# Optimization experiments

Measured on AMD Instinct MI355X. Metric: run time of the kernel, lower is better.

The kernel has to match this reference:

```python
import jax, jax.numpy as jnp
import numpy as np

B, N, DIM = 4, 4096, 512
HEADS, DH = 8, 64          # dim_head = dim // 8
M = 256                    # num_landmarks = dim // 2
ITERS = 6                  # pinv iterations
K = 33                     # residual depthwise conv kernel
INNER = HEADS * DH


def setup_inputs() -> dict:
    key = jax.random.key(0)
    ks = jax.random.split(key, 7)
    return {
        "x": jax.random.normal(ks[0], (B, N, DIM), jnp.float32),
        "norm_w": 1.0 + 0.02 * jax.random.normal(ks[1], (DIM,), jnp.float32),
        "norm_b": 0.02 * jax.random.normal(ks[2], (DIM,), jnp.float32),
        "w_qkv": jax.random.normal(ks[3], (DIM, 3 * INNER), jnp.float32) / np.sqrt(DIM),
        "w_out": jax.random.normal(ks[4], (INNER, DIM), jnp.float32) / np.sqrt(INNER),
        "b_out": 0.02 * jax.random.normal(ks[5], (DIM,), jnp.float32),
        "res_w": jax.random.normal(ks[6], (HEADS, 1, K, 1), jnp.float32) / np.sqrt(K),
    }


def _moore_penrose_pinv(x, iters):
    # iterative Newton-Schulz pseudoinverse, as in lucidrains nystrom-attention
    abs_x = jnp.abs(x)
    col = abs_x.sum(-1)
    row = abs_x.sum(-2)
    z = jnp.swapaxes(x, -1, -2) / (jnp.max(col) * jnp.max(row))
    I = jnp.eye(x.shape[-1], dtype=x.dtype)
    for _ in range(iters):
        xz = x @ z
        z = 0.25 * z @ (13.0 * I - xz @ (15.0 * I - xz @ (7.0 * I - xz)))
    return z


def reference(x, norm_w, norm_b, w_qkv, w_out, b_out, res_w):
    # LayerNorm (eps=1e-5, torch default)
    mu = x.mean(-1, keepdims=True)
    var = ((x - mu) ** 2).mean(-1, keepdims=True)
    xn = (x - mu) / jnp.sqrt(var + 1e-5) * norm_w + norm_b

    qkv = xn @ w_qkv                               # [B,N,3*INNER]
    q, k, v = jnp.split(qkv, 3, axis=-1)
    to_heads = lambda t: t.reshape(B, N, HEADS, DH).transpose(0, 2, 1, 3)  # [B,H,N,D]
    q, k, v = to_heads(q), to_heads(k), to_heads(v)
    q = q * (DH ** -0.5)

    # landmarks: mean over consecutive blocks of l = N // M tokens
    l = N // M
    q_l = q.reshape(B, HEADS, M, l, DH).mean(3)    # [B,H,M,D]
    k_l = k.reshape(B, HEADS, M, l, DH).mean(3)

    sim1 = jnp.einsum('bhid,bhjd->bhij', q, k_l)   # [B,H,N,M]
    sim2 = jnp.einsum('bhid,bhjd->bhij', q_l, k_l) # [B,H,M,M]
    sim3 = jnp.einsum('bhid,bhjd->bhij', q_l, k)   # [B,H,M,N]
    a1 = jax.nn.softmax(sim1, -1)
    a2 = jax.nn.softmax(sim2, -1)
    a3 = jax.nn.softmax(sim3, -1)

    a2_inv = _moore_penrose_pinv(a2, ITERS)
    out = (a1 @ a2_inv) @ (a3 @ v)                 # [B,H,N,D]

    # residual depthwise conv over sequence dim (Conv2d(h,h,(33,1),groups=h))
    out = out + jax.lax.conv_general_dilated(
        v, res_w, (1, 1), ((K // 2, K // 2), (0, 0)),
        feature_group_count=HEADS,
        dimension_numbers=('NCHW', 'OIHW', 'NCHW'))

    out = out.transpose(0, 2, 1, 3).reshape(B, N, INNER)
    out = out @ w_out + b_out                      # to_out (dropout inactive at eval)
    return x + out                                 # TransLayer residual
```

## Files before the change

kernel.cpp:

```cpp
#include <hip/hip_runtime.h>
#include <math.h>

typedef unsigned short u16;
typedef short s16x8 __attribute__((ext_vector_type(8)));
typedef float f32x4 __attribute__((ext_vector_type(4)));

#define MFMA16(a, b, c) __builtin_amdgcn_mfma_f32_16x16x32_bf16((a), (b), (c), 0, 0, 0)

__device__ __forceinline__ u16 f2b(float f) {
  unsigned u = __float_as_uint(f);
  unsigned r = (u + 0x7fff + ((u >> 16) & 1)) >> 16;
  return (u16)r;
}
__device__ __forceinline__ float b2f(u16 h) { return __uint_as_float(((unsigned)h) << 16); }

__global__ __launch_bounds__(256) void prep_kernel(const float* __restrict__ x, const float* __restrict__ w,
    const float* __restrict__ b, u16* __restrict__ xn,
    const float* __restrict__ Wq, u16* __restrict__ WqT,
    const float* __restrict__ Wo, u16* __restrict__ WoT,
    unsigned* __restrict__ scal) {
  int bI = blockIdx.x;
  int t = threadIdx.x;
  if (bI == 0 && t == 0) { scal[0] = 0u; scal[1] = 0u; }
  if (bI < 16384) {
    int row = bI;
    const float* xr = x + (size_t)row * 512;
    float v0 = xr[t], v1 = xr[t + 256];
    float s = v0 + v1, ss = v0*v0 + v1*v1;
    for (int o = 32; o > 0; o >>= 1) { s += __shfl_down(s, o); ss += __shfl_down(ss, o); }
    __shared__ float ls[4], lss[4];
    int wid = t >> 6, lane = t & 63;
    if (lane == 0) { ls[wid] = s; lss[wid] = ss; }
    __syncthreads();
    float tot  = ls[0]+ls[1]+ls[2]+ls[3];
    float tot2 = lss[0]+lss[1]+lss[2]+lss[3];
    float mean = tot * (1.f/512);
    float var  = tot2 * (1.f/512) - mean*mean;
    float inv = rsqrtf(var + 1e-5f);
    u16* xo = xn + (size_t)row * 512;
    xo[t]     = f2b((v0-mean)*inv*w[t]     + b[t]);
    xo[t+256] = f2b((v1-mean)*inv*w[t+256] + b[t+256]);
  } else if (bI < 16384 + 3072) {
    int idx = (bI - 16384)*256 + t;
    int r = idx / 1536, c = idx - r*1536;
    WqT[(size_t)c*512 + r] = f2b(Wq[idx]);
  } else {
    int idx = (bI - 19456)*256 + t;
    int r = idx >> 9, c = idx & 511;
    WoT[(size_t)c*512 + r] = f2b(Wo[idx]);
  }
}

__device__ __forceinline__ void gemm128_pf(const u16* __restrict__ A, const u16* __restrict__ BT,
    int K, int ldA, int ldBT, int row0, int col0, u16* As, u16* Bs, f32x4 acc[4][4]) {
  int t = threadIdx.x, lane = t & 63, wid = t >> 6;
  int wr = (wid >> 1) * 64, wc = (wid & 1) * 64;
  int lr = lane & 15, lg = lane >> 4;
  int sr = t >> 2, sc = (t & 3) * 8;
  const u16* Ar0 = A  + (size_t)(row0 + sr)*ldA + sc;
  const u16* Ar1 = A  + (size_t)(row0 + sr + 64)*ldA + sc;
  const u16* Br0 = BT + (size_t)(col0 + sr)*ldBT + sc;
  const u16* Br1 = BT + (size_t)(col0 + sr + 64)*ldBT + sc;
  uint4 pa0 = *(const uint4*)Ar0, pa1 = *(const uint4*)Ar1;
  uint4 pb0 = *(const uint4*)Br0, pb1 = *(const uint4*)Br1;
  for (int k0 = 0; k0 < K; k0 += 32) {
    __syncthreads();
    *(uint4*)&As[sr*40 + sc]        = pa0;
    *(uint4*)&As[(sr + 64)*40 + sc] = pa1;
    *(uint4*)&Bs[sr*40 + sc]        = pb0;
    *(uint4*)&Bs[(sr + 64)*40 + sc] = pb1;
    __syncthreads();
    if (k0 + 32 < K) {
      pa0 = *(const uint4*)(Ar0 + k0 + 32);
      pa1 = *(const uint4*)(Ar1 + k0 + 32);
      pb0 = *(const uint4*)(Br0 + k0 + 32);
      pb1 = *(const uint4*)(Br1 + k0 + 32);
    }
    s16x8 af[4], bf[4];
    #pragma unroll
    for (int f = 0; f < 4; f++) {
      af[f] = *(s16x8*)&As[(wr + f*16 + lr)*40 + lg*8];
      bf[f] = *(s16x8*)&Bs[(wc + f*16 + lr)*40 + lg*8];
    }
    #pragma unroll
    for (int i = 0; i < 4; i++)
      #pragma unroll
      for (int j = 0; j < 4; j++)
        acc[i][j] = MFMA16(af[i], bf[j], acc[i][j]);
  }
}

__device__ __forceinline__ void gemm64_pf(const u16* __restrict__ Ab, const u16* __restrict__ Bb,
    int row0, int col0, u16* As, u16* Bs, f32x4 acc[2][2]) {
  int t = threadIdx.x, lane = t & 63, wid = t >> 6;
  int wr = (wid >> 1)*32, wc = (wid & 1)*32;
  int lr = lane & 15, lg = lane >> 4;
  int sr = t >> 3, sc = (t & 7)*8;
  const u16* Ar0 = Ab + (size_t)(row0 + sr)*256 + sc;
  const u16* Ar1 = Ab + (size_t)(row0 + 32 + sr)*256 + sc;
  const u16* Br0 = Bb + (size_t)(col0 + sr)*256 + sc;
  const u16* Br1 = Bb + (size_t)(col0 + 32 + sr)*256 + sc;
  uint4 pa0 = *(const uint4*)Ar0, pa1 = *(const uint4*)Ar1;
  uint4 pb0 = *(const uint4*)Br0, pb1 = *(const uint4*)Br1;
  for (int k0 = 0; k0 < 256; k0 += 64) {
    __syncthreads();
    *(uint4*)&As[sr*72 + sc]        = pa0;
    *(uint4*)&As[(sr + 32)*72 + sc] = pa1;
    *(uint4*)&Bs[sr*72 + sc]        = pb0;
    *(uint4*)&Bs[(sr + 32)*72 + sc] = pb1;
    __syncthreads();
    if (k0 + 64 < 256) {
      pa0 = *(const uint4*)(Ar0 + k0 + 64);
      pa1 = *(const uint4*)(Ar1 + k0 + 64);
      pb0 = *(const uint4*)(Br0 + k0 + 64);
      pb1 = *(const uint4*)(Br1 + k0 + 64);
    }
    #pragma unroll
    for (int kk = 0; kk < 2; kk++) {
      s16x8 af[2], bf[2];
      #pragma unroll
      for (int f = 0; f < 2; f++) {
        af[f] = *(s16x8*)&As[(wr + f*16 + lr)*72 + kk*32 + lg*8];
        bf[f] = *(s16x8*)&Bs[(wc + f*16 + lr)*72 + kk*32 + lg*8];
      }
      #pragma unroll
      for (int i = 0; i < 2; i++)
        #pragma unroll
        for (int j = 0; j < 2; j++)
          acc[i][j] = MFMA16(af[i], bf[j], acc[i][j]);
    }
  }
}

__global__ __launch_bounds__(256, 4) void qkv_mfma(const u16* __restrict__ xn, const u16* __restrict__ wT,
    u16* __restrict__ q, u16* __restrict__ k, u16* __restrict__ v,
    u16* __restrict__ ql, u16* __restrict__ kl) {
  __shared__ u16 As[128*40], Bs[128*40];
  f32x4 acc[4][4];
  #pragma unroll
  for (int i = 0; i < 4; i++)
    #pragma unroll
    for (int j = 0; j < 4; j++) acc[i][j] = (f32x4)0.f;
  int bI = blockIdx.x;
  int job = (bI & 7)*192 + (bI >> 3);
  int row0 = (job / 12) * 128, col0 = (job % 12) * 128;
  gemm128_pf(xn, wT, 512, 512, 512, row0, col0, As, Bs, acc);
  int t = threadIdx.x, lane = t & 63, wid = t >> 6, lr = lane & 15, lg = lane >> 4;
  int wr = (wid >> 1)*64, wc = (wid & 1)*64;
  int part = col0 >> 9;
  #pragma unroll
  for (int i = 0; i < 4; i++)
    #pragma unroll
    for (int j = 0; j < 4; j++)
      #pragma unroll
      for (int r = 0; r < 4; r++) {
        int row = row0 + wr + i*16 + lg*4 + r;
        int col = col0 + wc + j*16 + lr;
        float val = acc[i][j][r];
        int rem = col & 511, h = rem >> 6, d = rem & 63;
        int b = row >> 12, n = row & 4095;
        size_t bh = (size_t)(b*8 + h);
        size_t dst = (bh*4096 + n)*64 + d;
        if (part == 0)      q[dst] = f2b(val * 0.125f);
        else if (part == 1) k[dst] = f2b(val);
        else                v[dst] = f2b(val);
      }
  if (part <= 1) {
    #pragma unroll
    for (int i = 0; i < 4; i++) {
      #pragma unroll
      for (int j = 0; j < 4; j++) {
        float s = acc[i][j][0] + acc[i][j][1] + acc[i][j][2] + acc[i][j][3];
        s += __shfl_xor(s, 16);
        s += __shfl_xor(s, 32);
        if (lg == 0) {
          int row16 = row0 + wr + i*16;
          int b = row16 >> 12, n = row16 & 4095;
          int m = n >> 4;
          int col = col0 + wc + j*16 + lr;
          int rem = col & 511, h = rem >> 6, d = rem & 63;
          size_t dst = ((size_t)(b*8 + h)*256 + m)*64 + d;
          if (part == 0) ql[dst] = f2b(s * (0.125f/16.f));
          else           kl[dst] = f2b(s * (1.f/16.f));
        }
      }
    }
  }
}

__global__ __launch_bounds__(256, 4) void out_mfma(const u16* __restrict__ outh, const u16* __restrict__ wT,
    const float* __restrict__ bo, const float* __restrict__ x, float* __restrict__ out) {
  __shared__ u16 As[128*40], Bs[128*40];
  f32x4 acc[4][4];
  #pragma unroll
  for (int i = 0; i < 4; i++)
    #pragma unroll
    for (int j = 0; j < 4; j++) acc[i][j] = (f32x4)0.f;
  int bI = blockIdx.x;
  int job = (bI & 7)*64 + (bI >> 3);
  int row0 = (job / 4) * 128, col0 = (job % 4) * 128;
  gemm128_pf(outh, wT, 512, 512, 512, row0, col0, As, Bs, acc);
  int t = threadIdx.x, lane = t & 63, wid = t >> 6, lr = lane & 15, lg = lane >> 4;
  int wr = (wid >> 1)*64, wc = (wid & 1)*64;
  #pragma unroll
  for (int i = 0; i < 4; i++)
    #pragma unroll
    for (int j = 0; j < 4; j++)
      #pragma unroll
      for (int r = 0; r < 4; r++) {
        int row = row0 + wr + i*16 + lg*4 + r;
        int col = col0 + wc + j*16 + lr;
        size_t idx = (size_t)row*512 + col;
        out[idx] = x[idx] + acc[i][j][r] + bo[col];
      }
}

__global__ __launch_bounds__(256) void mid_kernel(
    const u16* __restrict__ v, u16* __restrict__ vT,
    const u16* __restrict__ ql, const u16* __restrict__ kl,
    u16* __restrict__ a2h, float* __restrict__ pcs,
    const float* __restrict__ rw, u16* __restrict__ outh) {
  __shared__ __align__(16) u16 smem[25600];
  int bI = blockIdx.x;
  int t = threadIdx.x;
  if (bI < 128) {
    int rq = bI & 3, bh = bI >> 2;
    u16* Qs  = smem;
    u16* Ks2 = smem + 4608;
    float* wcol = (float*)(smem + 23040);
    int lane = t & 63, wid = t >> 6, lr = lane & 15, lg = lane >> 4;
    #pragma unroll
    for (int p = 0; p < 2; p++) {
      int c = t + p*256;
      int r = c >> 3, col = (c & 7)*8;
      *(uint4*)&Qs[r*72 + col] = *(const uint4*)&ql[((size_t)bh*256 + rq*64 + r)*64 + col];
    }
    #pragma unroll
    for (int p = 0; p < 8; p++) {
      int c = t + p*256;
      int r = c >> 3, col = (c & 7)*8;
      *(uint4*)&Ks2[r*72 + col] = *(const uint4*)&kl[((size_t)bh*256 + r)*64 + col];
    }
    __syncthreads();
    float colp[16];
    #pragma unroll
    for (int cf = 0; cf < 16; cf++) colp[cf] = 0.f;
    int rbase = wid*16;
    s16x8 a0 = *(s16x8*)&Qs[(rbase + lr)*72 + lg*8];
    s16x8 a1 = *(s16x8*)&Qs[(rbase + lr)*72 + 32 + lg*8];
    f32x4 sf[16];
    #pragma unroll
    for (int cf = 0; cf < 16; cf++) {
      s16x8 b0 = *(s16x8*)&Ks2[(cf*16 + lr)*72 + lg*8];
      s16x8 b1 = *(s16x8*)&Ks2[(cf*16 + lr)*72 + 32 + lg*8];
      sf[cf] = MFMA16(a1, b1, MFMA16(a0, b0, (f32x4)0.f));
    }
    #pragma unroll
    for (int r = 0; r < 4; r++) {
      float mx = -3e38f;
      #pragma unroll
      for (int cf = 0; cf < 16; cf++) mx = fmaxf(mx, sf[cf][r]);
      #pragma unroll
      for (int o = 1; o < 16; o <<= 1) mx = fmaxf(mx, __shfl_xor(mx, o));
      float sum = 0.f;
      #pragma unroll
      for (int cf = 0; cf < 16; cf++) { sf[cf][r] = __expf(sf[cf][r] - mx); sum += sf[cf][r]; }
      #pragma unroll
      for (int o = 1; o < 16; o <<= 1) sum += __shfl_xor(sum, o);
      float inv = 1.f / sum;
      int row = rq*64 + rbase + lg*4 + r;
      size_t base = (size_t)bh*65536 + (size_t)row*256;
      #pragma unroll
      for (int cf = 0; cf < 16; cf++) {
        float pp = sf[cf][r] * inv;
        a2h[base + cf*16 + lr] = f2b(pp);
        colp[cf] += pp;
      }
    }
    #pragma unroll
    for (int cf = 0; cf < 16; cf++) {
      colp[cf] += __shfl_xor(colp[cf], 16);
      colp[cf] += __shfl_xor(colp[cf], 32);
    }
    if (lg == 0) {
      #pragma unroll
      for (int cf = 0; cf < 16; cf++) wcol[wid*256 + cf*16 + lr] = colp[cf];
    }
    __syncthreads();
    pcs[((size_t)bh*4 + rq)*256 + t] = wcol[t] + wcol[256 + t] + wcol[512 + t] + wcol[768 + t];
  } else if (bI < 2176) {
    int idx = bI - 128;
    int bh = idx >> 6, n0 = (idx & 63) * 64;
    u16* tile = smem;
    const u16* vb = v + ((size_t)bh*4096 + n0)*64;
    #pragma unroll
    for (int p = 0; p < 2; p++) {
      int c = t + p*256;
      int r = c >> 3, col = (c & 7)*8;
      *(uint4*)&tile[r*72 + col] = *(const uint4*)&vb[(size_t)r*64 + col];
    }
    __syncthreads();
    #pragma unroll
    for (int p = 0; p < 2; p++) {
      int c = t + p*256;
      int d = c >> 3, ncol = (c & 7)*8;
      u16 tmp[8];
      #pragma unroll
      for (int j = 0; j < 8; j++) tmp[j] = tile[(ncol + j)*72 + d];
      *(uint4*)&vT[((size_t)bh*64 + d)*4096 + n0 + ncol] = *(uint4*)tmp;
    }
  } else {
    int idx = bI - 2176;
    int bh = idx >> 5, n0 = (idx & 31) * 128;
    int b = bh >> 3, h = bh & 7;
    u16* tile = smem;
    float* wsm = (float*)(smem + 11520);
    if (t < 33) wsm[t] = rw[h*33 + t];
    const u16* vb = v + ((size_t)bh*4096)*64;
    #pragma unroll
    for (int p = 0; p < 5; p++) {
      int c = t + p*256;
      int r = c >> 3, col = (c & 7)*8;
      int nn = n0 - 16 + r;
      uint4 val = make_uint4(0u,0u,0u,0u);
      if (nn >= 0 && nn < 4096) val = *(const uint4*)&vb[(size_t)nn*64 + col];
      *(uint4*)&tile[r*72 + col] = val;
    }
    __syncthreads();
    int d8 = (t & 7) * 8;
    int r0 = t >> 3;
    #pragma unroll
    for (int pass = 0; pass < 4; pass++) {
      int lrow = pass*32 + r0;
      float acc[8] = {};
      #pragma unroll
      for (int j = 0; j < 33; j++) {
        uint4 vv = *(uint4*)&tile[(lrow + j)*72 + d8];
        float w = wsm[j];
        acc[0] += b2f((u16)(vv.x & 0xffff)) * w;
        acc[1] += b2f((u16)(vv.x >> 16))    * w;
        acc[2] += b2f((u16)(vv.y & 0xffff)) * w;
        acc[3] += b2f((u16)(vv.y >> 16))    * w;
        acc[4] += b2f((u16)(vv.z & 0xffff)) * w;
        acc[5] += b2f((u16)(vv.z >> 16))    * w;
        acc[6] += b2f((u16)(vv.w & 0xffff)) * w;
        acc[7] += b2f((u16)(vv.w >> 16))    * w;
      }
      size_t oi = ((size_t)(b*4096 + n0 + lrow))*512 + h*64 + d8;
      uint4 nv;
      nv.x = (unsigned)f2b(acc[0]) | ((unsigned)f2b(acc[1]) << 16);
      nv.y = (unsigned)f2b(acc[2]) | ((unsigned)f2b(acc[3]) << 16);
      nv.z = (unsigned)f2b(acc[4]) | ((unsigned)f2b(acc[5]) << 16);
      nv.w = (unsigned)f2b(acc[6]) | ((unsigned)f2b(acc[7]) << 16);
      *(uint4*)&outh[oi] = nv;
    }
  }
}

__global__ __launch_bounds__(256) void colmax_kernel(const float* __restrict__ pcs, unsigned* __restrict__ scal) {
  __shared__ float red[256];
  int bh = blockIdx.x, t = threadIdx.x;
  size_t b4 = (size_t)bh*4*256;
  red[t] = pcs[b4 + t] + pcs[b4 + 256 + t] + pcs[b4 + 512 + t] + pcs[b4 + 768 + t];
  __syncthreads();
  for (int o = 128; o > 0; o >>= 1) {
    if (t < o) red[t] = fmaxf(red[t], red[t+o]);
    __syncthreads();
  }
  if (t == 0) atomicMax(scal + 1, __float_as_uint(red[0]));
}

__global__ __launch_bounds__(256) void flash_part(const u16* __restrict__ Q, const u16* __restrict__ Kg,
    const u16* __restrict__ VT, u16* __restrict__ po, float* __restrict__ pl) {
  __shared__ u16 Ks[64*72];
  __shared__ u16 Vs[64*72];
  __shared__ u16 Ps[4*16*72];
  int ch = blockIdx.x, qg = blockIdx.y, bh = blockIdx.z;
  int t = threadIdx.x, lane = t & 63, wid = t >> 6, lr = lane & 15, lg = lane >> 4;
  const u16* Qb  = Q  + ((size_t)bh*256)*64;
  const u16* Kb  = Kg + ((size_t)bh*4096 + ch*512)*64;
  const u16* VTb = VT + ((size_t)bh*64)*4096 + ch*512;
  s16x8 aq[2][2];
  #pragma unroll
  for (int qq = 0; qq < 2; qq++) {
    int qrow = (qg*2 + qq)*64 + wid*16 + lr;
    aq[qq][0] = *(const s16x8*)&Qb[(size_t)qrow*64 + lg*8];
    aq[qq][1] = *(const s16x8*)&Qb[(size_t)qrow*64 + 32 + lg*8];
  }
  f32x4 oacc[2][4];
  f32x4 lacc[2];
  #pragma unroll
  for (int qq = 0; qq < 2; qq++) {
    lacc[qq] = (f32x4)0.f;
    #pragma unroll
    for (int f = 0; f < 4; f++) oacc[qq][f] = (f32x4)0.f;
  }
  u16* Pw = Ps + wid*16*72;
  uint4 pk[2], pv[2];
  #pragma unroll
  for (int p = 0; p < 2; p++) {
    int c = t + p*256; int r = c >> 3, cc = (c & 7)*8;
    pk[p] = *(const uint4*)&Kb[(size_t)r*64 + cc];
    pv[p] = *(const uint4*)&VTb[(size_t)r*4096 + cc];
  }
  for (int k0 = 0; k0 < 512; k0 += 64) {
    __syncthreads();
    #pragma unroll
    for (int p = 0; p < 2; p++) {
      int c = t + p*256; int r = c >> 3, cc = (c & 7)*8;
      *(uint4*)&Ks[r*72 + cc] = pk[p];
      *(uint4*)&Vs[r*72 + cc] = pv[p];
    }
    __syncthreads();
    if (k0 + 64 < 512) {
      #pragma unroll
      for (int p = 0; p < 2; p++) {
        int c = t + p*256; int r = c >> 3, cc = (c & 7)*8;
        pk[p] = *(const uint4*)&Kb[(size_t)(k0 + 64 + r)*64 + cc];
        pv[p] = *(const uint4*)&VTb[(size_t)r*4096 + k0 + 64 + cc];
      }
    }
    #pragma unroll
    for (int qq = 0; qq < 2; qq++) {
      f32x4 sf[4];
      #pragma unroll
      for (int f = 0; f < 4; f++) {
        s16x8 b0 = *(s16x8*)&Ks[(f*16 + lr)*72 + lg*8];
        s16x8 b1 = *(s16x8*)&Ks[(f*16 + lr)*72 + 32 + lg*8];
        f32x4 s = (f32x4)0.f;
        s = MFMA16(aq[qq][0], b0, s);
        s = MFMA16(aq[qq][1], b1, s);
        sf[f] = s;
      }
      #pragma unroll
      for (int r = 0; r < 4; r++) {
        #pragma unroll
        for (int f = 0; f < 4; f++) {
          float pv2 = __expf(sf[f][r] - 8.f);
          lacc[qq][r] += pv2;
          Pw[(lg*4 + r)*72 + f*16 + lr] = f2b(pv2);
        }
      }
      #pragma unroll
      for (int ks = 0; ks < 2; ks++) {
        s16x8 ap = *(s16x8*)&Pw[lr*72 + ks*32 + lg*8];
        #pragma unroll
        for (int df = 0; df < 4; df++) {
          s16x8 bv = *(s16x8*)&Vs[(df*16 + lr)*72 + ks*32 + lg*8];
          oacc[qq][df] = MFMA16(ap, bv, oacc[qq][df]);
        }
      }
    }
  }
  #pragma unroll
  for (int qq = 0; qq < 2; qq++) {
    #pragma unroll
    for (int r = 0; r < 4; r++) {
      float s = lacc[qq][r];
      #pragma unroll
      for (int o = 1; o < 16; o <<= 1) s += __shfl_xor(s, o);
      lacc[qq][r] = s;
    }
  }
  #pragma unroll
  for (int qq = 0; qq < 2; qq++) {
    int pidx = (bh*4 + qg*2 + qq)*8 + ch;
    #pragma unroll
    for (int r = 0; r < 4; r++) {
      int lrow = wid*16 + lg*4 + r;
      if (lr == 0) pl[pidx*64 + lrow] = lacc[qq][r];
      uint2 pw2;
      pw2.x = (unsigned)f2b(oacc[qq][0][r]) | ((unsigned)f2b(oacc[qq][1][r]) << 16);
      pw2.y = (unsigned)f2b(oacc[qq][2][r]) | ((unsigned)f2b(oacc[qq][3][r]) << 16);
      *(uint2*)&po[((size_t)pidx*64 + lrow)*64 + lr*4] = pw2;
    }
  }
}

__global__ __launch_bounds__(256) void merge_z0(const u16* __restrict__ po,
    const float* __restrict__ pl, u16* __restrict__ a3vT,
    const u16* __restrict__ a2h, const unsigned* __restrict__ scal,
    u16* __restrict__ zA, u16* __restrict__ zAT) {
  __shared__ u16 tile[64*72];
  int bI = blockIdx.x;
  int t = threadIdx.x;
  if (bI < 128) {
    int qt = bI & 3, bh = bI >> 2;
    int lrow = t & 63, dg = t >> 6;
    int pbase = (bh*4 + qt)*8;
    float L = 0.f;
    #pragma unroll
    for (int ch = 0; ch < 8; ch++) L += pl[(pbase+ch)*64 + lrow];
    float Oacc[16];
    #pragma unroll
    for (int ss = 0; ss < 16; ss++) Oacc[ss] = 0.f;
    #pragma unroll
    for (int ch = 0; ch < 8; ch++) {
      const u16* pr = &po[(((size_t)(pbase+ch)*64 + lrow)*64) + dg*16];
      uint4 v0 = *(const uint4*)pr;
      uint4 v1 = *(const uint4*)(pr + 8);
      unsigned arr[8] = {v0.x, v0.y, v0.z, v0.w, v1.x, v1.y, v1.z, v1.w};
      #pragma unroll
      for (int jj = 0; jj < 8; jj++) {
        Oacc[jj*2]   += b2f((u16)(arr[jj] & 0xffff));
        Oacc[jj*2+1] += b2f((u16)(arr[jj] >> 16));
      }
    }
    float Linv = 1.f / L;
    #pragma unroll
    for (int ss = 0; ss < 16; ss++) {
      int s = dg*16 + ss;
      int c = ((s & 3) << 4) | (s >> 2);
      tile[c*72 + lrow] = f2b(Oacc[ss] * Linv);
    }
    __syncthreads();
    #pragma unroll
    for (int p = 0; p < 2; p++) {
      int idx = t + p*256;
      int d = idx >> 3, seg = idx & 7;
      u16 tmp[8];
      #pragma unroll
      for (int j = 0; j < 8; j++) tmp[j] = tile[d*72 + seg*8 + j];
      *(uint4*)&a3vT[((size_t)bh*64 + d)*256 + qt*64 + seg*8] = *(uint4*)tmp;
    }
  } else {
    size_t idx = (size_t)(bI - 128)*256 + t;
    float inv = 1.f / __uint_as_float(scal[1]);
    size_t bh = idx >> 16; int rem = (int)(idx & 65535); int i = rem >> 8, j = rem & 255;
    zA[idx]  = f2b(b2f(a2h[(bh<<16) + ((size_t)j<<8) + i]) * inv);
    zAT[idx] = f2b(b2f(a2h[idx]) * inv);
  }
}

__global__ __launch_bounds__(256) void pinv_s1(const u16* __restrict__ a2h, const u16* __restrict__ zcT,
    u16* __restrict__ xz, u16* __restrict__ xzT, u16* __restrict__ e1T) {
  __shared__ u16 As[64*72], Bs[64*72];
  size_t bb = (size_t)blockIdx.z << 16;
  f32x4 acc[2][2];
  #pragma unroll
  for (int i = 0; i < 2; i++) { acc[i][0] = (f32x4)0.f; acc[i][1] = (f32x4)0.f; }
  int row0 = blockIdx.y*64, col0 = blockIdx.x*64;
  gemm64_pf(a2h + bb, zcT + bb, row0, col0, As, Bs, acc);
  int t = threadIdx.x, lane = t & 63, wid = t >> 6, lr = lane & 15, lg = lane >> 4;
  int wr = (wid >> 1)*32, wc = (wid & 1)*32;
  #pragma unroll
  for (int i = 0; i < 2; i++)
    #pragma unroll
    for (int j = 0; j < 2; j++)
      #pragma unroll
      for (int r = 0; r < 4; r++) {
        int row = row0 + wr + i*16 + lg*4 + r;
        int col = col0 + wc + j*16 + lr;
        float c = acc[i][j][r];
        xz [bb + (size_t)row*256 + col] = f2b(c);
        xzT[bb + (size_t)col*256 + row] = f2b(c);
        e1T[bb + (size_t)col*256 + row] = f2b((row == col ? 7.f : 0.f) - c);
      }
}

__global__ __launch_bounds__(256) void pinv_s2(const u16* __restrict__ xz, const u16* __restrict__ e1T,
    const u16* __restrict__ zc, const u16* __restrict__ xzT,
    u16* __restrict__ e2T, u16* __restrict__ W) {
  __shared__ u16 As[64*72], Bs[64*72];
  int bz = blockIdx.z;
  bool isQ = bz < 32;
  size_t bb = (size_t)(isQ ? bz : bz - 32) << 16;
  const u16* Aptr = (isQ ? xz : zc) + bb;
  const u16* Bptr = (isQ ? e1T : xzT) + bb;
  f32x4 acc[2][2];
  #pragma unroll
  for (int i = 0; i < 2; i++) { acc[i][0] = (f32x4)0.f; acc[i][1] = (f32x4)0.f; }
  int row0 = blockIdx.y*64, col0 = blockIdx.x*64;
  gemm64_pf(Aptr, Bptr, row0, col0, As, Bs, acc);
  int t = threadIdx.x, lane = t & 63, wid = t >> 6, lr = lane & 15, lg = lane >> 4;
  int wr = (wid >> 1)*32, wc = (wid & 1)*32;
  #pragma unroll
  for (int i = 0; i < 2; i++)
    #pragma unroll
    for (int j = 0; j < 2; j++)
      #pragma unroll
      for (int r = 0; r < 4; r++) {
        int row = row0 + wr + i*16 + lg*4 + r;
        int col = col0 + wc + j*16 + lr;
        float c = acc[i][j][r];
        if (isQ) e2T[bb + (size_t)col*256 + row] = f2b((row == col ? 15.f : 0.f) - c);
        else     W  [bb + (size_t)row*256 + col] = f2b(c);
      }
}

__global__ __launch_bounds__(256) void pinv_s3(const u16* __restrict__ W, const u16* __restrict__ e2T,
    const u16* __restrict__ zc, u16* __restrict__ zn, u16* __restrict__ znT) {
  __shared__ u16 As[64*72], Bs[64*72];
  size_t bb = (size_t)blockIdx.z << 16;
  f32x4 acc[2][2];
  #pragma unroll
  for (int i = 0; i < 2; i++) { acc[i][0] = (f32x4)0.f; acc[i][1] = (f32x4)0.f; }
  int row0 = blockIdx.y*64, col0 = blockIdx.x*64;
  gemm64_pf(W + bb, e2T + bb, row0, col0, As, Bs, acc);
  int t = threadIdx.x, lane = t & 63, wid = t >> 6, lr = lane & 15, lg = lane >> 4;
  int wr = (wid >> 1)*32, wc = (wid & 1)*32;
  #pragma unroll
  for (int i = 0; i < 2; i++)
    #pragma unroll
    for (int j = 0; j < 2; j++)
      #pragma unroll
      for (int r = 0; r < 4; r++) {
        int row = row0 + wr + i*16 + lg*4 + r;
        int col = col0 + wc + j*16 + lr;
        size_t idx = bb + (size_t)row*256 + col;
        float val = 3.25f*b2f(zc[idx]) - 0.25f*acc[i][j][r];
        zn [idx] = f2b(val);
        znT[bb + (size_t)col*256 + row] = f2b(val);
      }
}

__global__ __launch_bounds__(256) void bmm64(const u16* __restrict__ A, const u16* __restrict__ BT,
    u16* __restrict__ CT, int M, int N, int K) {
  __shared__ u16 As[64*40], Bs[64*40];
  int batch = blockIdx.z;
  const u16* Ab = A  + (size_t)batch*M*K;
  const u16* Bb = BT + (size_t)batch*N*K;
  int row0 = blockIdx.y*64, col0 = blockIdx.x*64;
  int t = threadIdx.x, lane = t & 63, wid = t >> 6, lr = lane & 15, lg = lane >> 4;
  int wr = (wid >> 1)*32, wc = (wid & 1)*32;
  int sr = t >> 2, sc = (t & 3)*8;
  const u16* Arow = Ab + (size_t)(row0 + sr)*K + sc;
  const u16* Brow = Bb + (size_t)(col0 + sr)*K + sc;
  uint4 pa = *(const uint4*)Arow;
  uint4 pb = *(const uint4*)Brow;
  f32x4 acc[2][2];
  #pragma unroll
  for (int i = 0; i < 2; i++)
    #pragma unroll
    for (int j = 0; j < 2; j++) acc[i][j] = (f32x4)0.f;
  for (int k0 = 0; k0 < K; k0 += 32) {
    __syncthreads();
    *(uint4*)&As[sr*40 + sc] = pa;
    *(uint4*)&Bs[sr*40 + sc] = pb;
    __syncthreads();
    if (k0 + 32 < K) {
      pa = *(const uint4*)(Arow + k0 + 32);
      pb = *(const uint4*)(Brow + k0 + 32);
    }
    s16x8 af[2], bf[2];
    #pragma unroll
    for (int f = 0; f < 2; f++) {
      af[f] = *(s16x8*)&As[(wr + f*16 + lr)*40 + lg*8];
      bf[f] = *(s16x8*)&Bs[(wc + f*16 + lr)*40 + lg*8];
    }
    #pragma unroll
    for (int i = 0; i < 2; i++)
      #pragma unroll
      for (int j = 0; j < 2; j++)
        acc[i][j] = MFMA16(af[i], bf[j], acc[i][j]);
  }
  size_t cb = (size_t)batch*M*N;
  #pragma unroll
  for (int i = 0; i < 2; i++)
    #pragma unroll
    for (int j = 0; j < 2; j++)
      #pragma unroll
      for (int r = 0; r < 4; r++) {
        int row = row0 + wr + i*16 + lg*4 + r;
        int col = col0 + wc + j*16 + lr;
        CT[cb + (size_t)col*M + row] = f2b(acc[i][j][r]);
      }
}

__global__ __launch_bounds__(256, 4) void flash_a1(const u16* __restrict__ Q, const u16* __restrict__ Kl,
    const u16* __restrict__ W2T, u16* __restrict__ outh) {
  __shared__ u16 Ks[64*72];
  __shared__ u16 Vs[64*264];
  __shared__ u16 Ps[4*16*264];
  int bh = blockIdx.y;
  int q0 = blockIdx.x * 64;
  int t = threadIdx.x, lane = t & 63, wid = t >> 6, lr = lane & 15, lg = lane >> 4;
  const u16* Qb = Q + ((size_t)bh*4096)*64;
  #pragma unroll
  for (int p = 0; p < 8; p++) {
    int c = t + p*256; int r = c >> 5, col = (c & 31)*8;
    *(uint4*)&Vs[r*264 + col] = *(const uint4*)&W2T[((size_t)bh*64 + r)*256 + col];
  }
  int qrow = q0 + wid*16 + lr;
  s16x8 aq0 = *(const s16x8*)&Qb[(size_t)qrow*64 + lg*8];
  s16x8 aq1 = *(const s16x8*)&Qb[(size_t)qrow*64 + 32 + lg*8];
  f32x4 sf[16];
  #pragma unroll
  for (int f = 0; f < 16; f++) sf[f] = (f32x4)0.f;
  #pragma unroll
  for (int kt = 0; kt < 4; kt++) {
    __syncthreads();
    #pragma unroll
    for (int p = 0; p < 2; p++) {
      int c = t + p*256; int r = c >> 3, cc = (c & 7)*8;
      *(uint4*)&Ks[r*72 + cc] = *(const uint4*)&Kl[((size_t)bh*256 + kt*64 + r)*64 + cc];
    }
    __syncthreads();
    #pragma unroll
    for (int f2 = 0; f2 < 4; f2++) {
      s16x8 b0 = *(s16x8*)&Ks[(f2*16 + lr)*72 + lg*8];
      s16x8 b1 = *(s16x8*)&Ks[(f2*16 + lr)*72 + 32 + lg*8];
      sf[kt*4 + f2] = MFMA16(aq1, b1, MFMA16(aq0, b0, sf[kt*4 + f2]));
    }
  }
  u16* Pw = Ps + wid*16*264;
  float linv[4];
  #pragma unroll
  for (int r = 0; r < 4; r++) {
    float sum = 0.f;
    #pragma unroll
    for (int f = 0; f < 16; f++) {
      float pv = __expf(sf[f][r] - 8.f);
      sum += pv;
      Pw[(lg*4 + r)*264 + f*16 + lr] = f2b(pv);
    }
    #pragma unroll
    for (int o = 1; o < 16; o <<= 1) sum += __shfl_xor(sum, o);
    linv[r] = 1.f / sum;
  }
  f32x4 oacc[4];
  #pragma unroll
  for (int f = 0; f < 4; f++) oacc[f] = (f32x4)0.f;
  #pragma unroll
  for (int ks = 0; ks < 8; ks++) {
    s16x8 ap = *(s16x8*)&Pw[lr*264 + ks*32 + lg*8];
    #pragma unroll
    for (int df = 0; df < 4; df++) {
      s16x8 bv = *(s16x8*)&Vs[(df*16 + lr)*264 + ks*32 + lg*8];
      oacc[df] = MFMA16(ap, bv, oacc[df]);
    }
  }
  int b = bh >> 3, h = bh & 7;
  #pragma unroll
  for (int df = 0; df < 4; df++)
    #pragma unroll
    for (int r = 0; r < 4; r++) {
      int lrow = wid*16 + lg*4 + r;
      int col = df*16 + lr;
      size_t oi = ((size_t)(b*4096 + q0 + lrow))*512 + h*64 + col;
      outh[oi] = f2b(b2f(outh[oi]) + oacc[df][r] * linv[r]);
    }
}

extern "C" void kernel_launch(void* const* d_in, const int* in_sizes, int n_in,
                              void* d_out, int out_size, void* d_ws, size_t ws_size,
                              hipStream_t stream) {
  const float* x      = (const float*)d_in[0];
  const float* norm_w = (const float*)d_in[1];
  const float* norm_b = (const float*)d_in[2];
  const float* w_qkv  = (const float*)d_in[3];
  const float* w_out  = (const float*)d_in[4];
  const float* b_out  = (const float*)d_in[5];
  const float* res_w  = (const float*)d_in[6];
  float* out = (float*)d_out;
  char* ws = (char*)d_ws;

  size_t off = 0;
  u16* xn    = (u16*)(ws + off); off += 16777216;
  u16* q     = (u16*)(ws + off); off += 16777216;
  u16* k     = (u16*)(ws + off); off += 16777216;
  u16* v     = (u16*)(ws + off); off += 16777216;
  u16* vT    = (u16*)(ws + off); off += 16777216;
  u16* ql    = (u16*)(ws + off); off += 1048576;
  u16* kl    = (u16*)(ws + off); off += 1048576;
  u16* a2h   = (u16*)(ws + off); off += 4194304;
  u16* zA    = (u16*)(ws + off); off += 4194304;
  u16* zAT   = (u16*)(ws + off); off += 4194304;
  u16* zB    = (u16*)(ws + off); off += 4194304;
  u16* zBT   = (u16*)(ws + off); off += 4194304;
  u16* xz    = (u16*)(ws + off); off += 4194304;
  u16* xzT   = (u16*)(ws + off); off += 4194304;
  u16* e1T   = (u16*)(ws + off); off += 4194304;
  u16* e2T   = (u16*)(ws + off); off += 4194304;
  u16* Wm    = (u16*)(ws + off); off += 4194304;
  u16* a3vT  = (u16*)(ws + off); off += 1048576;
  u16* w2T   = (u16*)(ws + off); off += 1048576;
  u16* wqkvT = (u16*)(ws + off); off += 1572864;
  u16* woutT = (u16*)(ws + off); off += 524288;
  u16* outh  = (u16*)(ws + off); off += 16777216;
  u16* po    = (u16*)(ws + off); off += 8388608;
  float* pl  = (float*)(ws + off); off += 262144;
  float* pcs = (float*)(ws + off); off += 131072;
  unsigned* scal = (unsigned*)(ws + off); off += 8;

  prep_kernel<<<20480, 256, 0, stream>>>(x, norm_w, norm_b, xn, w_qkv, wqkvT, w_out, woutT, scal);
  qkv_mfma<<<1536, 256, 0, stream>>>(xn, wqkvT, q, k, v, ql, kl);
  mid_kernel<<<3200, 256, 0, stream>>>(v, vT, ql, kl, a2h, pcs, res_w, outh);
  colmax_kernel<<<32, 256, 0, stream>>>(pcs, scal);
  flash_part<<<dim3(8, 2, 32), 256, 0, stream>>>(ql, k, vT, po, pl);
  merge_z0<<<8320, 256, 0, stream>>>(po, pl, a3vT, a2h, scal, zA, zAT);

  u16 *zc = zA, *zcT = zAT, *zn = zB, *znT = zBT;
  for (int it = 0; it < 6; it++) {
    pinv_s1<<<dim3(4,4,32), 256, 0, stream>>>(a2h, zcT, xz, xzT, e1T);
    pinv_s2<<<dim3(4,4,64), 256, 0, stream>>>(xz, e1T, zc, xzT, e2T, Wm);
    pinv_s3<<<dim3(4,4,32), 256, 0, stream>>>(Wm, e2T, zc, zn, znT);
    u16* tp;
    tp = zc; zc = zn; zn = tp;
    tp = zcT; zcT = znT; znT = tp;
  }

  bmm64<<<dim3(1,4,32), 256, 0, stream>>>(zc, a3vT, w2T, 256, 64, 256);
  flash_a1<<<dim3(64, 32), 256, 0, stream>>>(q, kl, w2T, outh);
  out_mfma<<<512, 256, 0, stream>>>(outh, woutT, b_out, x, out);
}
```

Measured before the change: 384.5 us.

## Load full K panel in one pass for 64x64 GEMMs and fuse colmax into flash_part

The 64x64 GEMM helper used by the pinv stages and bmm64 now loads the entire 256-wide K panel into shared memory in one pass behind a single barrier. This replaces the register-prefetched loop that synchronised on every K chunk. The colmax reduction is folded into the flash_part launch as extra blocks, removing one kernel launch. The trade-off is about 67 KB of shared memory per block, which lowers occupancy and leaves no overlap between the loads and the MFMA work.

```diff
diff --git a/kernel.cpp b/kernel.cpp
--- a/kernel.cpp
+++ b/kernel.cpp
@@ -90,45 +90,32 @@
   }
 }
 
-__device__ __forceinline__ void gemm64_pf(const u16* __restrict__ Ab, const u16* __restrict__ Bb,
+__device__ __forceinline__ void gemm64_1p(const u16* __restrict__ Ab, const u16* __restrict__ Bb,
     int row0, int col0, u16* As, u16* Bs, f32x4 acc[2][2]) {
   int t = threadIdx.x, lane = t & 63, wid = t >> 6;
   int wr = (wid >> 1)*32, wc = (wid & 1)*32;
   int lr = lane & 15, lg = lane >> 4;
-  int sr = t >> 3, sc = (t & 7)*8;
-  const u16* Ar0 = Ab + (size_t)(row0 + sr)*256 + sc;
-  const u16* Ar1 = Ab + (size_t)(row0 + 32 + sr)*256 + sc;
-  const u16* Br0 = Bb + (size_t)(col0 + sr)*256 + sc;
-  const u16* Br1 = Bb + (size_t)(col0 + 32 + sr)*256 + sc;
-  uint4 pa0 = *(const uint4*)Ar0, pa1 = *(const uint4*)Ar1;
-  uint4 pb0 = *(const uint4*)Br0, pb1 = *(const uint4*)Br1;
-  for (int k0 = 0; k0 < 256; k0 += 64) {
-    __syncthreads();
-    *(uint4*)&As[sr*72 + sc]        = pa0;
-    *(uint4*)&As[(sr + 32)*72 + sc] = pa1;
-    *(uint4*)&Bs[sr*72 + sc]        = pb0;
-    *(uint4*)&Bs[(sr + 32)*72 + sc] = pb1;
-    __syncthreads();
-    if (k0 + 64 < 256) {
-      pa0 = *(const uint4*)(Ar0 + k0 + 64);
-      pa1 = *(const uint4*)(Ar1 + k0 + 64);
-      pb0 = *(const uint4*)(Br0 + k0 + 64);
-      pb1 = *(const uint4*)(Br1 + k0 + 64);
-    }
-    #pragma unroll
-    for (int kk = 0; kk < 2; kk++) {
-      s16x8 af[2], bf[2];
-      #pragma unroll
-      for (int f = 0; f < 2; f++) {
-        af[f] = *(s16x8*)&As[(wr + f*16 + lr)*72 + kk*32 + lg*8];
-        bf[f] = *(s16x8*)&Bs[(wc + f*16 + lr)*72 + kk*32 + lg*8];
-      }
-      #pragma unroll
-      for (int i = 0; i < 2; i++)
-        #pragma unroll
-        for (int j = 0; j < 2; j++)
-          acc[i][j] = MFMA16(af[i], bf[j], acc[i][j]);
-    }
+  #pragma unroll
+  for (int p = 0; p < 8; p++) {
+    int idx = t + p*256;
+    int r = idx >> 5, c = (idx & 31)*8;
+    *(uint4*)&As[r*264 + c] = *(const uint4*)&Ab[(size_t)(row0 + r)*256 + c];
+    *(uint4*)&Bs[r*264 + c] = *(const uint4*)&Bb[(size_t)(col0 + r)*256 + c];
+  }
+  __syncthreads();
+  #pragma unroll
+  for (int kk = 0; kk < 8; kk++) {
+    s16x8 af[2], bf[2];
+    #pragma unroll
+    for (int f = 0; f < 2; f++) {
+      af[f] = *(s16x8*)&As[(wr + f*16 + lr)*264 + kk*32 + lg*8];
+      bf[f] = *(s16x8*)&Bs[(wc + f*16 + lr)*264 + kk*32 + lg*8];
+    }
+    #pragma unroll
+    for (int i = 0; i < 2; i++)
+      #pragma unroll
+      for (int j = 0; j < 2; j++)
+        acc[i][j] = MFMA16(af[i], bf[j], acc[i][j]);
   }
 }
 
@@ -357,26 +344,30 @@
   }
 }
 
-__global__ __launch_bounds__(256) void colmax_kernel(const float* __restrict__ pcs, unsigned* __restrict__ scal) {
-  __shared__ float red[256];
-  int bh = blockIdx.x, t = threadIdx.x;
-  size_t b4 = (size_t)bh*4*256;
-  red[t] = pcs[b4 + t] + pcs[b4 + 256 + t] + pcs[b4 + 512 + t] + pcs[b4 + 768 + t];
-  __syncthreads();
-  for (int o = 128; o > 0; o >>= 1) {
-    if (t < o) red[t] = fmaxf(red[t], red[t+o]);
-    __syncthreads();
-  }
-  if (t == 0) atomicMax(scal + 1, __float_as_uint(red[0]));
-}
-
-__global__ __launch_bounds__(256) void flash_part(const u16* __restrict__ Q, const u16* __restrict__ Kg,
-    const u16* __restrict__ VT, u16* __restrict__ po, float* __restrict__ pl) {
-  __shared__ u16 Ks[64*72];
-  __shared__ u16 Vs[64*72];
-  __shared__ u16 Ps[4*16*72];
-  int ch = blockIdx.x, qg = blockIdx.y, bh = blockIdx.z;
-  int t = threadIdx.x, lane = t & 63, wid = t >> 6, lr = lane & 15, lg = lane >> 4;
+__global__ __launch_bounds__(256) void fp_cm(const u16* __restrict__ Q, const u16* __restrict__ Kg,
+    const u16* __restrict__ VT, u16* __restrict__ po, float* __restrict__ pl,
+    const float* __restrict__ pcs, unsigned* __restrict__ scal) {
+  __shared__ __align__(16) u16 smem[13824];
+  int bI = blockIdx.x;
+  int t = threadIdx.x;
+  if (bI >= 512) {
+    float* red = (float*)smem;
+    int bh = bI - 512;
+    size_t b4 = (size_t)bh*4*256;
+    red[t] = pcs[b4 + t] + pcs[b4 + 256 + t] + pcs[b4 + 512 + t] + pcs[b4 + 768 + t];
+    __syncthreads();
+    for (int o = 128; o > 0; o >>= 1) {
+      if (t < o) red[t] = fmaxf(red[t], red[t+o]);
+      __syncthreads();
+    }
+    if (t == 0) atomicMax(scal + 1, __float_as_uint(red[0]));
+    return;
+  }
+  int ch = bI & 7, qg = (bI >> 3) & 1, bh = bI >> 4;
+  u16* Ks = smem;
+  u16* Vs = smem + 4608;
+  u16* Ps = smem + 9216;
+  int lane = t & 63, wid = t >> 6, lr = lane & 15, lg = lane >> 4;
   const u16* Qb  = Q  + ((size_t)bh*256)*64;
   const u16* Kb  = Kg + ((size_t)bh*4096 + ch*512)*64;
   const u16* VTb = VT + ((size_t)bh*64)*4096 + ch*512;
@@ -534,13 +525,13 @@
 
 __global__ __launch_bounds__(256) void pinv_s1(const u16* __restrict__ a2h, const u16* __restrict__ zcT,
     u16* __restrict__ xz, u16* __restrict__ xzT, u16* __restrict__ e1T) {
-  __shared__ u16 As[64*72], Bs[64*72];
+  __shared__ u16 As[64*264], Bs[64*264];
   size_t bb = (size_t)blockIdx.z << 16;
   f32x4 acc[2][2];
   #pragma unroll
   for (int i = 0; i < 2; i++) { acc[i][0] = (f32x4)0.f; acc[i][1] = (f32x4)0.f; }
   int row0 = blockIdx.y*64, col0 = blockIdx.x*64;
-  gemm64_pf(a2h + bb, zcT + bb, row0, col0, As, Bs, acc);
+  gemm64_1p(a2h + bb, zcT + bb, row0, col0, As, Bs, acc);
   int t = threadIdx.x, lane = t & 63, wid = t >> 6, lr = lane & 15, lg = lane >> 4;
   int wr = (wid >> 1)*32, wc = (wid & 1)*32;
   #pragma unroll
@@ -561,7 +552,7 @@
 __global__ __launch_bounds__(256) void pinv_s2(const u16* __restrict__ xz, const u16* __restrict__ e1T,
     const u16* __restrict__ zc, const u16* __restrict__ xzT,
     u16* __restrict__ e2T, u16* __restrict__ W) {
-  __shared__ u16 As[64*72], Bs[64*72];
+  __shared__ u16 As[64*264], Bs[64*264];
   int bz = blockIdx.z;
   bool isQ = bz < 32;
   size_t bb = (size_t)(isQ ? bz : bz - 32) << 16;
@@ -571,7 +562,7 @@
   #pragma unroll
   for (int i = 0; i < 2; i++) { acc[i][0] = (f32x4)0.f; acc[i][1] = (f32x4)0.f; }
   int row0 = blockIdx.y*64, col0 = blockIdx.x*64;
-  gemm64_pf(Aptr, Bptr, row0, col0, As, Bs, acc);
+  gemm64_1p(Aptr, Bptr, row0, col0, As, Bs, acc);
   int t = threadIdx.x, lane = t & 63, wid = t >> 6, lr = lane & 15, lg = lane >> 4;
   int wr = (wid >> 1)*32, wc = (wid & 1)*32;
   #pragma unroll
@@ -590,13 +581,13 @@
 
 __global__ __launch_bounds__(256) void pinv_s3(const u16* __restrict__ W, const u16* __restrict__ e2T,
     const u16* __restrict__ zc, u16* __restrict__ zn, u16* __restrict__ znT) {
-  __shared__ u16 As[64*72], Bs[64*72];
+  __shared__ u16 As[64*264], Bs[64*264];
   size_t bb = (size_t)blockIdx.z << 16;
   f32x4 acc[2][2];
   #pragma unroll
   for (int i = 0; i < 2; i++) { acc[i][0] = (f32x4)0.f; acc[i][1] = (f32x4)0.f; }
   int row0 = blockIdx.y*64, col0 = blockIdx.x*64;
-  gemm64_pf(W + bb, e2T + bb, row0, col0, As, Bs, acc);
+  gemm64_1p(W + bb, e2T + bb, row0, col0, As, Bs, acc);
   int t = threadIdx.x, lane = t & 63, wid = t >> 6, lr = lane & 15, lg = lane >> 4;
   int wr = (wid >> 1)*32, wc = (wid & 1)*32;
   #pragma unroll
@@ -616,44 +607,17 @@
 
 __global__ __launch_bounds__(256) void bmm64(const u16* __restrict__ A, const u16* __restrict__ BT,
     u16* __restrict__ CT, int M, int N, int K) {
-  __shared__ u16 As[64*40], Bs[64*40];
+  __shared__ u16 As[64*264], Bs[64*264];
   int batch = blockIdx.z;
   const u16* Ab = A  + (size_t)batch*M*K;
   const u16* Bb = BT + (size_t)batch*N*K;
   int row0 = blockIdx.y*64, col0 = blockIdx.x*64;
+  f32x4 acc[2][2];
+  #pragma unroll
+  for (int i = 0; i < 2; i++) { acc[i][0] = (f32x4)0.f; acc[i][1] = (f32x4)0.f; }
+  gemm64_1p(Ab, Bb, row0, col0, As, Bs, acc);
   int t = threadIdx.x, lane = t & 63, wid = t >> 6, lr = lane & 15, lg = lane >> 4;
   int wr = (wid >> 1)*32, wc = (wid & 1)*32;
-  int sr = t >> 2, sc = (t & 3)*8;
-  const u16* Arow = Ab + (size_t)(row0 + sr)*K + sc;
-  const u16* Brow = Bb + (size_t)(col0 + sr)*K + sc;
-  uint4 pa = *(const uint4*)Arow;
-  uint4 pb = *(const uint4*)Brow;
-  f32x4 acc[2][2];
-  #pragma unroll
-  for (int i = 0; i < 2; i++)
-    #pragma unroll
-    for (int j = 0; j < 2; j++) acc[i][j] = (f32x4)0.f;
-  for (int k0 = 0; k0 < K; k0 += 32) {
-    __syncthreads();
-    *(uint4*)&As[sr*40 + sc] = pa;
-    *(uint4*)&Bs[sr*40 + sc] = pb;
-    __syncthreads();
-    if (k0 + 32 < K) {
-      pa = *(const uint4*)(Arow + k0 + 32);
-      pb = *(const uint4*)(Brow + k0 + 32);
-    }
-    s16x8 af[2], bf[2];
-    #pragma unroll
-    for (int f = 0; f < 2; f++) {
-      af[f] = *(s16x8*)&As[(wr + f*16 + lr)*40 + lg*8];
-      bf[f] = *(s16x8*)&Bs[(wc + f*16 + lr)*40 + lg*8];
-    }
-    #pragma unroll
-    for (int i = 0; i < 2; i++)
-      #pragma unroll
-      for (int j = 0; j < 2; j++)
-        acc[i][j] = MFMA16(af[i], bf[j], acc[i][j]);
-  }
   size_t cb = (size_t)batch*M*N;
   #pragma unroll
   for (int i = 0; i < 2; i++)
@@ -786,8 +750,7 @@
   prep_kernel<<<20480, 256, 0, stream>>>(x, norm_w, norm_b, xn, w_qkv, wqkvT, w_out, woutT, scal);
   qkv_mfma<<<1536, 256, 0, stream>>>(xn, wqkvT, q, k, v, ql, kl);
   mid_kernel<<<3200, 256, 0, stream>>>(v, vT, ql, kl, a2h, pcs, res_w, outh);
-  colmax_kernel<<<32, 256, 0, stream>>>(pcs, scal);
-  flash_part<<<dim3(8, 2, 32), 256, 0, stream>>>(ql, k, vT, po, pl);
+  fp_cm<<<544, 256, 0, stream>>>(ql, k, vT, po, pl, pcs, scal);
   merge_z0<<<8320, 256, 0, stream>>>(po, pl, a3vT, a2h, scal, zA, zAT);
 
   u16 *zc = zA, *zcT = zAT, *zn = zB, *znT = zBT;
```

Measured after the change: 395.7 us. 1.03x slower.
